# Performance work log

Hardware: AMD Instinct MI355X
Metric: run time of the kernel (lower is better)

The kernel has to match this reference:

```python
import jax, jax.numpy as jnp
import numpy as np

B, S, D = 2, 2048, 1024
H = 16
HD = D // H  # 64
SCALE = HD ** -0.5
EPS = 1e-12  # F.normalize eps


def _rope_sin_cos(length, half, dtype):
    positions = jnp.arange(length, dtype=dtype)
    freqs = jnp.arange(half, dtype=dtype)
    inv_freq = 1.0 / 10000 ** (freqs / max(1, half))
    theta = jnp.einsum('s,f->sf', positions, inv_freq)  # [S, half]
    return jnp.sin(theta)[None, None], jnp.cos(theta)[None, None]  # [1,1,S,half]


def _rotate(x, sin, cos):
    # x: [B,H,S,HD]; interleaved even/odd rotation
    x_even = x[..., 0::2]
    x_odd = x[..., 1::2]
    r_even = x_even * cos - x_odd * sin
    r_odd = x_even * sin + x_odd * cos
    return jnp.stack([r_even, r_odd], axis=-1).reshape(x.shape)


def setup_inputs() -> dict:
    key = jax.random.key(0)
    k1, k2, k3 = jax.random.split(key, 3)
    tokens = jax.random.normal(k1, (B, S, D), dtype=jnp.float32)
    qkv_w = jax.random.normal(k2, (3 * D, D), dtype=jnp.float32) * (D ** -0.5)
    qkv_b = jnp.zeros((3 * D,), dtype=jnp.float32)
    out_w = jax.random.normal(k3, (D, D), dtype=jnp.float32) * (D ** -0.5)
    out_b = jnp.zeros((D,), dtype=jnp.float32)
    return {"tokens": tokens, "qkv_w": qkv_w, "qkv_b": qkv_b,
            "out_w": out_w, "out_b": out_b}


def reference(tokens, qkv_w, qkv_b, out_w, out_b):
    batch, length, _ = tokens.shape
    qkv = tokens @ qkv_w.T + qkv_b                       # [B,S,3D]
    qkv = qkv.reshape(batch, length, 3, H, HD)
    qkv = jnp.transpose(qkv, (0, 3, 1, 2, 4))            # [B,H,S,3,HD]
    q, k, v = qkv[..., 0, :], qkv[..., 1, :], qkv[..., 2, :]
    sin, cos = _rope_sin_cos(length, HD // 2, q.dtype)
    q = _rotate(q, sin, cos)
    k = _rotate(k, sin, cos)
    # QK L2-normalize (F.normalize: x / max(||x||, eps))
    q = q / jnp.maximum(jnp.linalg.norm(q, axis=-1, keepdims=True), EPS)
    k = k / jnp.maximum(jnp.linalg.norm(k, axis=-1, keepdims=True), EPS)
    scores = jnp.einsum('bhqd,bhkd->bhqk', q, k) * SCALE
    attn = jax.nn.softmax(scores, axis=-1)
    out = jnp.einsum('bhqk,bhkd->bhqd', attn, v)          # [B,H,S,HD]
    out = jnp.transpose(out, (0, 2, 1, 3)).reshape(batch, length, D)
    return out @ out_w.T + out_b
```

## Files before the change

kernel.cpp:

```cpp
#include <hip/hip_runtime.h>
#include <hip/hip_bf16.h>
#include <math.h>

#define B_ 2
#define S_ 2048
#define D_ 1024
#define H_ 16
#define HD_ 64
#define BHS (B_*H_*S_)
#define NROWS (B_*S_)

typedef __attribute__((ext_vector_type(8))) short bf16x8;
typedef __attribute__((ext_vector_type(4))) short bf16x4;
typedef __attribute__((ext_vector_type(4))) float f32x4;
typedef __attribute__((ext_vector_type(4))) int i32x4;

#ifdef __HIP_DEVICE_COMPILE__
#define EXP2(x) __builtin_amdgcn_exp2f(x)
#else
#define EXP2(x) exp2f(x)
#endif

#define MFMA32(a, b, c) __builtin_amdgcn_mfma_f32_16x16x32_bf16(a, b, c, 0, 0, 0)

#define SCALE_LOG2E 0.18033688011112043f

#define VMCNT(N) asm volatile("s_waitcnt vmcnt(" #N ")" ::: "memory")
#define SBAR() do { __builtin_amdgcn_s_barrier(); \
                    __builtin_amdgcn_sched_barrier(0); } while (0)
#define SCHED0() __builtin_amdgcn_sched_barrier(0)

__device__ __forceinline__ short f2bf(float x) {
  __hip_bfloat16 h = __float2bfloat16(x);
  return *reinterpret_cast<short*>(&h);
}
__device__ __forceinline__ int packbf_hu(float lo, float hi) {
  unsigned lb = __float_as_uint(lo) + 0x8000u;
  unsigned hb = __float_as_uint(hi) + 0x8000u;
  return (int)__builtin_amdgcn_perm(hb, lb, 0x07060302u);
}

__device__ __forceinline__ void gload_lds16(const short* g, short* l) {
  __builtin_amdgcn_global_load_lds(
      (const __attribute__((address_space(1))) void*)g,
      (__attribute__((address_space(3))) void*)l, 16, 0, 0);
}

__global__ __launch_bounds__(256) void prep(
    const float* __restrict__ tokens, const float* __restrict__ qkv_w,
    const float* __restrict__ out_w, short* __restrict__ tok_bf,
    short* __restrict__ qkvw_bf, short* __restrict__ outw_bf,
    float* __restrict__ tab) {
  const int i = blockIdx.x * 256 + threadIdx.x;
  const float* src;
  short* dst;
  int j;
  if (i < 524288) {
    src = tokens; dst = tok_bf; j = i;
  } else if (i < 917504) {
    src = qkv_w; dst = qkvw_bf; j = i - 524288;
  } else if (i < 1048576) {
    src = out_w; dst = outw_bf; j = i - 917504;
  } else if (i < 1056768) {
    const int e = (i - 1048576) * 8;
    const int s = e >> 5;
    const int f0 = e & 31;
#pragma unroll
    for (int k = 0; k < 8; k++) {
      const int f = f0 + k;
      const float theta = (float)s * exp2f(-(float)f * 0.41524101186092034f);
      float sn, cs;
      sincosf(theta, &sn, &cs);
      tab[(s * 32 + f) * 2] = sn;
      tab[(s * 32 + f) * 2 + 1] = cs;
    }
    return;
  } else {
    return;
  }
  const float4 a = *(const float4*)(src + (long)j * 8);
  const float4 b = *(const float4*)(src + (long)j * 8 + 4);
  short tmp[8] = {f2bf(a.x), f2bf(a.y), f2bf(a.z), f2bf(a.w),
                  f2bf(b.x), f2bf(b.y), f2bf(b.z), f2bf(b.w)};
  *(bf16x8*)(dst + (long)j * 8) = *(const bf16x8*)tmp;
}

__global__ __launch_bounds__(256) void qkv_mfma(
    const short* __restrict__ A, const short* __restrict__ W,
    const float* __restrict__ bias, const float* __restrict__ tab,
    short* __restrict__ qb, short* __restrict__ kb, short* __restrict__ vtb) {
  __shared__ short smem[32768];
  const int t = threadIdx.x;
  const int w = t >> 6;
  const int lane = t & 63;
  const int col = lane & 15;
  const int quad = lane >> 4;
  const int wm = w >> 1;
  const int wn = w & 1;
  const int bid = blockIdx.x;
  const int xcd = bid & 7;
  const int seq = bid >> 3;
  const int m0 = (seq / 3) * 128;
  const int n0 = (xcd * 3 + seq % 3) * 128;

  f32x4 acc[4][4] = {};

  auto stage = [&](short* As, short* Bs, int k0) {
#pragma unroll
    for (int i = 0; i < 4; i++) {
      const int c0 = i * 256 + w * 64;
      const int c = c0 + lane;
      const int row = c >> 3;
      const int gseg = (c & 7) ^ (row & 7);
      gload_lds16(&A[(m0 + row) * 1024 + k0 + gseg * 8], As + c0 * 8);
    }
#pragma unroll
    for (int i = 0; i < 4; i++) {
      const int c0 = i * 256 + w * 64;
      const int c = c0 + lane;
      const int row = c >> 3;
      const int gseg = (c & 7) ^ (row & 7);
      gload_lds16(&W[(n0 + row) * 1024 + k0 + gseg * 8], Bs + c0 * 8);
    }
  };

  auto compute = [&](const short* As, const short* Bs) {
#pragma unroll
    for (int half = 0; half < 2; half++) {
      bf16x8 af[4], bfr[4];
#pragma unroll
      for (int mt = 0; mt < 4; mt++) {
        const int m = wm * 64 + mt * 16 + col;
        af[mt] =
            *(const bf16x8*)&As[m * 64 + (((quad + half * 4) ^ (m & 7)) * 8)];
      }
#pragma unroll
      for (int nt = 0; nt < 4; nt++) {
        const int n = wn * 64 + nt * 16 + col;
        bfr[nt] =
            *(const bf16x8*)&Bs[n * 64 + (((quad + half * 4) ^ (n & 7)) * 8)];
      }
#pragma unroll
      for (int mt = 0; mt < 4; mt++)
#pragma unroll
        for (int nt = 0; nt < 4; nt++)
          acc[mt][nt] = MFMA32(af[mt], bfr[nt], acc[mt][nt]);
    }
  };

  short* As0 = smem;          short* Bs0 = smem + 8192;
  short* As1 = smem + 16384;  short* Bs1 = smem + 24576;

  stage(As0, Bs0, 0);
  for (int it = 0; it < 8; it++) {
    const int k = it * 128;
    VMCNT(0); SBAR();
    stage(As1, Bs1, k + 64);
    SCHED0();
    compute(As0, Bs0);
    VMCNT(0); SBAR();
    if (it < 7) stage(As0, Bs0, k + 128);
    SCHED0();
    compute(As1, Bs1);
  }
  __syncthreads();

  const int j_base = n0 + wn * 64;
  const int c = j_base >> 10;
  const int h = (j_base >> 6) & 15;
  float bi[4];
#pragma unroll
  for (int nt = 0; nt < 4; nt++) bi[nt] = bias[j_base + nt * 16 + col];

  if (c < 2) {
    short* dst = (c == 0) ? qb : kb;
    float* Tf = (float*)smem + w * 1088;
#pragma unroll
    for (int mt = 0; mt < 4; mt++) {
#pragma unroll
      for (int nt = 0; nt < 4; nt++)
#pragma unroll
        for (int r = 0; r < 4; r++)
          Tf[(quad * 4 + r) * 68 + nt * 16 + col] = acc[mt][nt][r] + bi[nt];
#pragma unroll
      for (int p = 0; p < 4; p++) {
        const int rloc = p * 4 + quad;
        const int n = m0 + wm * 64 + mt * 16 + rloc;
        const int bidx = n >> 11;
        const int s = n & 2047;
        const float4 xv = *(const float4*)&Tf[rloc * 68 + col * 4];
        const float4 tc = *(const float4*)&tab[s * 64 + col * 4];
        const float e0 = xv.x * tc.y - xv.y * tc.x;
        const float o0 = xv.x * tc.x + xv.y * tc.y;
        const float e1 = xv.z * tc.w - xv.w * tc.z;
        const float o1 = xv.z * tc.z + xv.w * tc.w;
        float ss = e0 * e0 + o0 * o0 + e1 * e1 + o1 * o1;
        ss += __shfl_xor(ss, 1, 64);
        ss += __shfl_xor(ss, 2, 64);
        ss += __shfl_xor(ss, 4, 64);
        ss += __shfl_xor(ss, 8, 64);
        float scl = 1.0f / fmaxf(sqrtf(ss), 1e-12f);
        if (c == 0) scl *= SCALE_LOG2E;
        int2 pk;
        pk.x = packbf_hu(e0 * scl, o0 * scl);
        pk.y = packbf_hu(e1 * scl, o1 * scl);
        *(int2*)&dst[((long)(bidx * 16 + h) * 2048 + s) * 64 + col * 4] = pk;
      }
    }
  } else {
    const int bidx = m0 >> 11;
    const int st = ((m0 & 2047) >> 6) + wm;
    short* vbase = vtb + ((long)(bidx * 16 + h) * 32 + st) * 4096;
#pragma unroll
    for (int mtp = 0; mtp < 2; mtp++)
#pragma unroll
      for (int ntq = 0; ntq < 4; ntq++) {
        int4 pk4;
        pk4.x = packbf_hu(acc[2 * mtp][ntq][0] + bi[ntq],
                          acc[2 * mtp][ntq][1] + bi[ntq]);
        pk4.y = packbf_hu(acc[2 * mtp][ntq][2] + bi[ntq],
                          acc[2 * mtp][ntq][3] + bi[ntq]);
        pk4.z = packbf_hu(acc[2 * mtp + 1][ntq][0] + bi[ntq],
                          acc[2 * mtp + 1][ntq][1] + bi[ntq]);
        pk4.w = packbf_hu(acc[2 * mtp + 1][ntq][2] + bi[ntq],
                          acc[2 * mtp + 1][ntq][3] + bi[ntq]);
        *(int4*)&vbase[(mtp * 4 + ntq) * 512 + quad * 128 + col * 8] = pk4;
      }
  }
}

__global__ __launch_bounds__(512) void attn_mfma(
    const short* __restrict__ qb,
    const short* __restrict__ kb,
    const short* __restrict__ vt,
    short* __restrict__ ob) {
  __shared__ __align__(16) char smem[65536];
  short* Ks = (short*)smem;
  short* Vs = Ks + 16384;
  const int t = threadIdx.x;
  const int w = t >> 6;
  const int grp = w >> 2;
  const int wl = w & 3;
  const int lane = t & 63;
  const int col = lane & 15;
  const int quad = lane >> 4;
  const int bh = blockIdx.x;
  const int q0 = blockIdx.y * 128;
  const long hb = (long)bh * S_ * 64;
  const short* kg = kb + hb;
  const short* vg = vt + (long)bh * 64 * S_;

  bf16x8 qa[2][2];
#pragma unroll
  for (int mt2 = 0; mt2 < 2; mt2++)
#pragma unroll
    for (int h = 0; h < 2; h++)
      qa[mt2][h] = *(const bf16x8*)&qb[hb +
          (long)(q0 + wl * 32 + mt2 * 16 + col) * 64 + h * 32 + quad * 8];

  const int tt = (wl << 6) | lane;
  int kofs[2];
#pragma unroll
  for (int i = 0; i < 2; i++) {
    const int cc = tt + 256 * i;
    kofs[i] = ((cc >> 7) * 16 + (cc & 15)) * 64 + ((cc >> 6) & 1) * 32 +
              ((cc >> 4) & 3) * 8;
  }

  short* KfL0 = Ks + grp * 4096;
  short* KfL1 = KfL0 + 8192;
  short* VfL0 = Vs + grp * 4096;
  short* VfL1 = VfL0 + 8192;

  f32x4 oacc[2][4] = {};
  f32x4 lacc[2] = {};
  const short oneb = 0x3F80;
  const bf16x8 ones8 = {oneb, oneb, oneb, oneb, oneb, oneb, oneb, oneb};

  auto stage = [&](short* KfL, short* VfL, int kt) {
    const short* kgp = kg + (long)kt * 64;
    const short* vgp = vg + (long)(kt >> 6) * 4096;
#pragma unroll
    for (int i = 0; i < 2; i++) {
      gload_lds16(kgp + kofs[i], KfL + i * 2048 + wl * 512);
      gload_lds16(vgp + (tt + 256 * i) * 8, VfL + i * 2048 + wl * 512);
    }
  };

  auto compute = [&](const short* KfL, const short* VfL) {
#pragma unroll
    for (int ntp = 0; ntp < 2; ntp++) {
      i32x4 pw[2];
#pragma unroll
      for (int half = 0; half < 2; half++) {
        const int nt = ntp * 2 + half;
        const bf16x8 ka0 =
            *(const bf16x8*)&KfL[nt * 1024 + quad * 128 + col * 8];
        const bf16x8 ka1 =
            *(const bf16x8*)&KfL[nt * 1024 + 512 + quad * 128 + col * 8];
#pragma unroll
        for (int mt2 = 0; mt2 < 2; mt2++) {
          f32x4 z = {0.f, 0.f, 0.f, 0.f};
          z = MFMA32(ka0, qa[mt2][0], z);
          z = MFMA32(ka1, qa[mt2][1], z);
          const float e0 = EXP2(z[0]);
          const float e1 = EXP2(z[1]);
          const float e2 = EXP2(z[2]);
          const float e3 = EXP2(z[3]);
          if (half == 0) {
            pw[mt2].x = packbf_hu(e0, e1);
            pw[mt2].y = packbf_hu(e2, e3);
          } else {
            pw[mt2].z = packbf_hu(e0, e1);
            pw[mt2].w = packbf_hu(e2, e3);
          }
        }
      }
      const bf16x8 pb0 = __builtin_bit_cast(bf16x8, pw[0]);
      const bf16x8 pb1 = __builtin_bit_cast(bf16x8, pw[1]);
      lacc[0] = MFMA32(ones8, pb0, lacc[0]);
      lacc[1] = MFMA32(ones8, pb1, lacc[1]);
      __builtin_amdgcn_s_setprio(1);
#pragma unroll
      for (int dt = 0; dt < 4; dt++) {
        const bf16x8 va = *(const bf16x8*)
            &VfL[(ntp * 4 + dt) * 512 + quad * 128 + col * 8];
        oacc[0][dt] = MFMA32(va, pb0, oacc[0][dt]);
        oacc[1][dt] = MFMA32(va, pb1, oacc[1][dt]);
      }
      __builtin_amdgcn_s_setprio(0);
    }
  };

  const int base = grp * 1024;
  stage(KfL0, VfL0, base);
  for (int it = 0; it < 8; it++) {
    const int kt0 = base + it * 128;
    VMCNT(0); SBAR();
    stage(KfL1, VfL1, kt0 + 64);
    SCHED0();
    compute(KfL0, VfL0);
    VMCNT(0); SBAR();
    if (it < 7) stage(KfL0, VfL0, kt0 + 128);
    SCHED0();
    compute(KfL1, VfL1);
  }
  __syncthreads();

  float* Ocomb = (float*)smem;
  float* lsumC = (float*)(smem + 34816);
  if (grp == 1) {
#pragma unroll
    for (int mt2 = 0; mt2 < 2; mt2++) {
      const int qloc = wl * 32 + mt2 * 16 + col;
      if (quad == 0) lsumC[qloc] = lacc[mt2][0];
#pragma unroll
      for (int dt = 0; dt < 4; dt++)
        *(f32x4*)&Ocomb[qloc * 68 + dt * 16 + quad * 4] = oacc[mt2][dt];
    }
  }
  __syncthreads();
  if (grp == 0) {
#pragma unroll
    for (int mt2 = 0; mt2 < 2; mt2++) {
      const int qloc = wl * 32 + mt2 * 16 + col;
      const float inv = 1.0f / (lacc[mt2][0] + lsumC[qloc]);
      short* orow = ob + hb + (long)(q0 + qloc) * 64;
#pragma unroll
      for (int dt = 0; dt < 4; dt++) {
        const float4 oc = *(const float4*)&Ocomb[qloc * 68 + dt * 16 + quad * 4];
        int2 pk;
        pk.x = packbf_hu((oacc[mt2][dt][0] + oc.x) * inv,
                         (oacc[mt2][dt][1] + oc.y) * inv);
        pk.y = packbf_hu((oacc[mt2][dt][2] + oc.z) * inv,
                         (oacc[mt2][dt][3] + oc.w) * inv);
        *(int2*)&orow[dt * 16 + quad * 4] = pk;
      }
    }
  }
}

__global__ __launch_bounds__(256) void out_mfma(
    const short* __restrict__ O, const short* __restrict__ W,
    const float* __restrict__ bias, float* __restrict__ out) {
  __shared__ short smem[16384];
  const int t = threadIdx.x;
  const int w = t >> 6;
  const int lane = t & 63;
  const int col = lane & 15;
  const int quad = lane >> 4;
  const int wm = w >> 1;
  const int wn = w & 1;
  const int bid = blockIdx.x;
  const int xcd = bid & 7;
  const int seq = bid >> 3;
  const int m0 = (seq >> 1) * 64;
  const int n0 = (xcd * 2 + (seq & 1)) * 64;

  f32x4 acc[2][2] = {};

  auto stage = [&](short* As, short* Bs, int k0) {
#pragma unroll
    for (int i = 0; i < 2; i++) {
      const int c0 = i * 256 + w * 64;
      const int c = c0 + lane;
      const int row = c >> 3;
      const int gseg = (c & 7) ^ (row & 7);
      const int n = m0 + row;
      const int bidx = n >> 11;
      const int s = n & 2047;
      const int kk = k0 + gseg * 8;
      gload_lds16(&O[((long)(bidx * 16 + (kk >> 6)) * 2048 + s) * 64 + (kk & 63)],
                  As + c0 * 8);
    }
#pragma unroll
    for (int i = 0; i < 2; i++) {
      const int c0 = i * 256 + w * 64;
      const int c = c0 + lane;
      const int row = c >> 3;
      const int gseg = (c & 7) ^ (row & 7);
      gload_lds16(&W[(n0 + row) * 1024 + k0 + gseg * 8], Bs + c0 * 8);
    }
  };

  auto compute = [&](const short* As, const short* Bs) {
#pragma unroll
    for (int half = 0; half < 2; half++) {
      bf16x8 af[2], bfr[2];
#pragma unroll
      for (int mt = 0; mt < 2; mt++) {
        const int m = wm * 32 + mt * 16 + col;
        af[mt] =
            *(const bf16x8*)&As[m * 64 + (((quad + half * 4) ^ (m & 7)) * 8)];
      }
#pragma unroll
      for (int nt = 0; nt < 2; nt++) {
        const int n = wn * 32 + nt * 16 + col;
        bfr[nt] =
            *(const bf16x8*)&Bs[n * 64 + (((quad + half * 4) ^ (n & 7)) * 8)];
      }
#pragma unroll
      for (int mt = 0; mt < 2; mt++)
#pragma unroll
        for (int nt = 0; nt < 2; nt++)
          acc[mt][nt] = MFMA32(af[mt], bfr[nt], acc[mt][nt]);
    }
  };

  short* As0 = smem;         short* Bs0 = smem + 4096;
  short* As1 = smem + 8192;  short* Bs1 = smem + 12288;

  stage(As0, Bs0, 0);
  for (int it = 0; it < 8; it++) {
    const int k = it * 128;
    VMCNT(0); SBAR();
    stage(As1, Bs1, k + 64);
    SCHED0();
    compute(As0, Bs0);
    VMCNT(0); SBAR();
    if (it < 7) stage(As0, Bs0, k + 128);
    SCHED0();
    compute(As1, Bs1);
  }

  float bi[2];
#pragma unroll
  for (int nt = 0; nt < 2; nt++) bi[nt] = bias[n0 + wn * 32 + nt * 16 + col];
#pragma unroll
  for (int mt = 0; mt < 2; mt++) {
#pragma unroll
    for (int r = 0; r < 4; r++) {
      const int n = m0 + wm * 32 + mt * 16 + quad * 4 + r;
#pragma unroll
      for (int nt = 0; nt < 2; nt++)
        out[(long)n * 1024 + n0 + wn * 32 + nt * 16 + col] =
            acc[mt][nt][r] + bi[nt];
    }
  }
}

extern "C" void kernel_launch(void* const* d_in, const int* in_sizes, int n_in,
                              void* d_out, int out_size, void* d_ws,
                              size_t ws_size, hipStream_t stream) {
  const float* tokens = (const float*)d_in[0];
  const float* qkv_w = (const float*)d_in[1];
  const float* qkv_b = (const float*)d_in[2];
  const float* out_w = (const float*)d_in[3];
  const float* out_b = (const float*)d_in[4];
  float* out = (float*)d_out;

  const size_t per = (size_t)BHS * HD_;
  float* tab = (float*)d_ws;
  short* tok_bf = (short*)(tab + 2048 * 64);
  short* qkvw_bf = tok_bf + per;
  short* outw_bf = qkvw_bf + 3 * per / 4;
  short* q_bf = outw_bf + per / 4;
  short* k_bf = q_bf + per;
  short* vt_bf = k_bf + per;
  short* O_bf = vt_bf + per;

  hipLaunchKernelGGL(prep, dim3(4128), dim3(256), 0, stream, tokens, qkv_w,
                     out_w, tok_bf, qkvw_bf, outw_bf, tab);
  hipLaunchKernelGGL(qkv_mfma, dim3(768), dim3(256), 0, stream, tok_bf,
                     qkvw_bf, qkv_b, tab, q_bf, k_bf, vt_bf);
  hipLaunchKernelGGL(attn_mfma, dim3(B_ * H_, S_ / 128), dim3(512), 0, stream,
                     q_bf, k_bf, vt_bf, O_bf);
  hipLaunchKernelGGL(out_mfma, dim3(1024), dim3(256), 0, stream, O_bf,
                     outw_bf, out_b, out);
}
```

Before: 175.8 us.

## Split attention KV range across four wave groups and remap blocks to XCDs

The attention kernel now runs 1024-thread blocks in which four groups of four waves each handle a quarter of the key range, using 32-key stage tiles instead of 64. Partial outputs and row sums are reduced through shared memory in three sequential steps. The grid is flattened to 1D and remapped so that all query blocks of a head land on the same XCD, aiming for better L2 reuse of K/V. More waves per block are meant to hide latency, at the cost of extra reduction barriers and smaller per-stage tiles.

```diff
diff --git a/kernel.cpp b/kernel.cpp
--- a/kernel.cpp
+++ b/kernel.cpp
@@ -229,7 +229,7 @@
   }
 }
 
-__global__ __launch_bounds__(512) void attn_mfma(
+__global__ __launch_bounds__(1024) void attn_mfma(
     const short* __restrict__ qb,
     const short* __restrict__ kb,
     const short* __restrict__ vt,
@@ -244,8 +244,11 @@
   const int lane = t & 63;
   const int col = lane & 15;
   const int quad = lane >> 4;
-  const int bh = blockIdx.x;
-  const int q0 = blockIdx.y * 128;
+  const int bid = blockIdx.x;
+  const int xcd = bid & 7;
+  const int j = bid >> 3;
+  const int bh = xcd * 4 + (j >> 4);
+  const int q0 = (j & 15) * 128;
   const long hb = (long)bh * S_ * 64;
   const short* kg = kb + hb;
   const short* vg = vt + (long)bh * 64 * S_;
@@ -259,17 +262,12 @@
           (long)(q0 + wl * 32 + mt2 * 16 + col) * 64 + h * 32 + quad * 8];
 
   const int tt = (wl << 6) | lane;
-  int kofs[2];
-#pragma unroll
-  for (int i = 0; i < 2; i++) {
-    const int cc = tt + 256 * i;
-    kofs[i] = ((cc >> 7) * 16 + (cc & 15)) * 64 + ((cc >> 6) & 1) * 32 +
-              ((cc >> 4) & 3) * 8;
-  }
-
-  short* KfL0 = Ks + grp * 4096;
+  const int kofs = ((tt >> 7) * 16 + (tt & 15)) * 64 + ((tt >> 6) & 1) * 32 +
+                   ((tt >> 4) & 3) * 8;
+
+  short* KfL0 = Ks + grp * 2048;
   short* KfL1 = KfL0 + 8192;
-  short* VfL0 = Vs + grp * 4096;
+  short* VfL0 = Vs + grp * 2048;
   short* VfL1 = VfL0 + 8192;
 
   f32x4 oacc[2][4] = {};
@@ -279,69 +277,62 @@
 
   auto stage = [&](short* KfL, short* VfL, int kt) {
     const short* kgp = kg + (long)kt * 64;
-    const short* vgp = vg + (long)(kt >> 6) * 4096;
-#pragma unroll
-    for (int i = 0; i < 2; i++) {
-      gload_lds16(kgp + kofs[i], KfL + i * 2048 + wl * 512);
-      gload_lds16(vgp + (tt + 256 * i) * 8, VfL + i * 2048 + wl * 512);
-    }
+    const short* vgp = vg + (long)(kt >> 6) * 4096 + ((kt >> 5) & 1) * 2048;
+    gload_lds16(kgp + kofs, KfL + wl * 512);
+    gload_lds16(vgp + tt * 8, VfL + wl * 512);
   };
 
   auto compute = [&](const short* KfL, const short* VfL) {
-#pragma unroll
-    for (int ntp = 0; ntp < 2; ntp++) {
-      i32x4 pw[2];
-#pragma unroll
-      for (int half = 0; half < 2; half++) {
-        const int nt = ntp * 2 + half;
-        const bf16x8 ka0 =
-            *(const bf16x8*)&KfL[nt * 1024 + quad * 128 + col * 8];
-        const bf16x8 ka1 =
-            *(const bf16x8*)&KfL[nt * 1024 + 512 + quad * 128 + col * 8];
-#pragma unroll
-        for (int mt2 = 0; mt2 < 2; mt2++) {
-          f32x4 z = {0.f, 0.f, 0.f, 0.f};
-          z = MFMA32(ka0, qa[mt2][0], z);
-          z = MFMA32(ka1, qa[mt2][1], z);
-          const float e0 = EXP2(z[0]);
-          const float e1 = EXP2(z[1]);
-          const float e2 = EXP2(z[2]);
-          const float e3 = EXP2(z[3]);
-          if (half == 0) {
-            pw[mt2].x = packbf_hu(e0, e1);
-            pw[mt2].y = packbf_hu(e2, e3);
-          } else {
-            pw[mt2].z = packbf_hu(e0, e1);
-            pw[mt2].w = packbf_hu(e2, e3);
-          }
+    i32x4 pw[2];
+#pragma unroll
+    for (int half = 0; half < 2; half++) {
+      const int nt = half;
+      const bf16x8 ka0 = *(const bf16x8*)&KfL[nt * 1024 + quad * 128 + col * 8];
+      const bf16x8 ka1 =
+          *(const bf16x8*)&KfL[nt * 1024 + 512 + quad * 128 + col * 8];
+#pragma unroll
+      for (int mt2 = 0; mt2 < 2; mt2++) {
+        f32x4 z = {0.f, 0.f, 0.f, 0.f};
+        z = MFMA32(ka0, qa[mt2][0], z);
+        z = MFMA32(ka1, qa[mt2][1], z);
+        const float e0 = EXP2(z[0]);
+        const float e1 = EXP2(z[1]);
+        const float e2 = EXP2(z[2]);
+        const float e3 = EXP2(z[3]);
+        if (half == 0) {
+          pw[mt2].x = packbf_hu(e0, e1);
+          pw[mt2].y = packbf_hu(e2, e3);
+        } else {
+          pw[mt2].z = packbf_hu(e0, e1);
+          pw[mt2].w = packbf_hu(e2, e3);
         }
       }
-      const bf16x8 pb0 = __builtin_bit_cast(bf16x8, pw[0]);
-      const bf16x8 pb1 = __builtin_bit_cast(bf16x8, pw[1]);
-      lacc[0] = MFMA32(ones8, pb0, lacc[0]);
-      lacc[1] = MFMA32(ones8, pb1, lacc[1]);
-      __builtin_amdgcn_s_setprio(1);
-#pragma unroll
-      for (int dt = 0; dt < 4; dt++) {
-        const bf16x8 va = *(const bf16x8*)
-            &VfL[(ntp * 4 + dt) * 512 + quad * 128 + col * 8];
-        oacc[0][dt] = MFMA32(va, pb0, oacc[0][dt]);
-        oacc[1][dt] = MFMA32(va, pb1, oacc[1][dt]);
-      }
-      __builtin_amdgcn_s_setprio(0);
-    }
+    }
+    const bf16x8 pb0 = __builtin_bit_cast(bf16x8, pw[0]);
+    const bf16x8 pb1 = __builtin_bit_cast(bf16x8, pw[1]);
+    lacc[0] = MFMA32(ones8, pb0, lacc[0]);
+    lacc[1] = MFMA32(ones8, pb1, lacc[1]);
+    __builtin_amdgcn_s_setprio(1);
+#pragma unroll
+    for (int dt = 0; dt < 4; dt++) {
+      const bf16x8 va =
+          *(const bf16x8*)&VfL[dt * 512 + quad * 128 + col * 8];
+      oacc[0][dt] = MFMA32(va, pb0, oacc[0][dt]);
+      oacc[1][dt] = MFMA32(va, pb1, oacc[1][dt]);
+    }
+    __builtin_amdgcn_s_setprio(0);
   };
 
-  const int base = grp * 1024;
+  const int base = grp * 512;
   stage(KfL0, VfL0, base);
   for (int it = 0; it < 8; it++) {
-    const int kt0 = base + it * 128;
+    const int kt0 = base + it * 64;
     VMCNT(0); SBAR();
-    stage(KfL1, VfL1, kt0 + 64);
+    stage(KfL1, VfL1, kt0 + 32);
     SCHED0();
     compute(KfL0, VfL0);
     VMCNT(0); SBAR();
-    if (it < 7) stage(KfL0, VfL0, kt0 + 128);
+    if (it < 7) stage(KfL0, VfL0, kt0 + 64);
     SCHED0();
     compute(KfL1, VfL1);
   }
@@ -349,7 +340,7 @@
 
   float* Ocomb = (float*)smem;
   float* lsumC = (float*)(smem + 34816);
-  if (grp == 1) {
+  if (grp == 3) {
 #pragma unroll
     for (int mt2 = 0; mt2 < 2; mt2++) {
       const int qloc = wl * 32 + mt2 * 16 + col;
@@ -357,6 +348,34 @@
 #pragma unroll
       for (int dt = 0; dt < 4; dt++)
         *(f32x4*)&Ocomb[qloc * 68 + dt * 16 + quad * 4] = oacc[mt2][dt];
+    }
+  }
+  __syncthreads();
+  if (grp == 2) {
+#pragma unroll
+    for (int mt2 = 0; mt2 < 2; mt2++) {
+      const int qloc = wl * 32 + mt2 * 16 + col;
+      if (quad == 0) lsumC[qloc] += lacc[mt2][0];
+#pragma unroll
+      for (int dt = 0; dt < 4; dt++) {
+        f32x4 v = *(const f32x4*)&Ocomb[qloc * 68 + dt * 16 + quad * 4];
+        v += oacc[mt2][dt];
+        *(f32x4*)&Ocomb[qloc * 68 + dt * 16 + quad * 4] = v;
+      }
+    }
+  }
+  __syncthreads();
+  if (grp == 1) {
+#pragma unroll
+    for (int mt2 = 0; mt2 < 2; mt2++) {
+      const int qloc = wl * 32 + mt2 * 16 + col;
+      if (quad == 0) lsumC[qloc] += lacc[mt2][0];
+#pragma unroll
+      for (int dt = 0; dt < 4; dt++) {
+        f32x4 v = *(const f32x4*)&Ocomb[qloc * 68 + dt * 16 + quad * 4];
+        v += oacc[mt2][dt];
+        *(f32x4*)&Ocomb[qloc * 68 + dt * 16 + quad * 4] = v;
+      }
     }
   }
   __syncthreads();
@@ -503,7 +522,7 @@
                      out_w, tok_bf, qkvw_bf, outw_bf, tab);
   hipLaunchKernelGGL(qkv_mfma, dim3(768), dim3(256), 0, stream, tok_bf,
                      qkvw_bf, qkv_b, tab, q_bf, k_bf, vt_bf);
-  hipLaunchKernelGGL(attn_mfma, dim3(B_ * H_, S_ / 128), dim3(512), 0, stream,
+  hipLaunchKernelGGL(attn_mfma, dim3(512), dim3(1024), 0, stream,
                      q_bf, k_bf, vt_bf, O_bf);
   hipLaunchKernelGGL(out_mfma, dim3(1024), dim3(256), 0, stream, O_bf,
                      outw_bf, out_b, out);
```

Result: slower. 182.5 us (+3.8%).
